# Kernel tuning notes

Hardware: AMD Instinct MI355X
Metric: run time of the kernel (lower is better)

The kernel has to match this reference:

```python
import jax, jax.numpy as jnp
import numpy as np

DIM = 1024
HEADS = 16
HEAD_DIM = DIM // HEADS
HIDDEN = 4 * DIM
EPS = 1e-6


def _layer_norm(x, scale, bias):
    mu = jnp.mean(x, axis=-1, keepdims=True)
    var = jnp.mean(jnp.square(x - mu), axis=-1, keepdims=True)
    return (x - mu) * jax.lax.rsqrt(var + EPS) * scale + bias


def setup_inputs() -> dict:
    key = jax.random.key(0)
    ks = jax.random.split(key, 8)
    s = 0.02
    return {
        "x": jax.random.normal(ks[0], (8, 1024, DIM), dtype=jnp.float32),
        "w_qkv": jax.random.normal(ks[1], (DIM, 3 * DIM), dtype=jnp.float32) * s,
        "b_qkv": jnp.zeros((3 * DIM,), jnp.float32),
        "w_proj": jax.random.normal(ks[2], (DIM, DIM), dtype=jnp.float32) * s,
        "b_proj": jnp.zeros((DIM,), jnp.float32),
        "ln1_scale": jnp.ones((DIM,), jnp.float32),
        "ln1_bias": jnp.zeros((DIM,), jnp.float32),
        "ln2_scale": jnp.ones((DIM,), jnp.float32),
        "ln2_bias": jnp.zeros((DIM,), jnp.float32),
        "w_fc1": jax.random.normal(ks[3], (DIM, HIDDEN), dtype=jnp.float32) * s,
        "b_fc1": jnp.zeros((HIDDEN,), jnp.float32),
        "w_fc2": jax.random.normal(ks[4], (HIDDEN, DIM), dtype=jnp.float32) * s,
        "b_fc2": jnp.zeros((DIM,), jnp.float32),
    }


def reference(x, w_qkv, b_qkv, w_proj, b_proj, ln1_scale, ln1_bias,
              ln2_scale, ln2_bias, w_fc1, b_fc1, w_fc2, b_fc2):
    B, N, C = x.shape
    scale = HEAD_DIM ** -0.5

    # --- attention branch ---
    h = _layer_norm(x, ln1_scale, ln1_bias)
    qkv = h @ w_qkv + b_qkv                          # [B,N,3C]
    qkv = qkv.reshape(B, N, 3, HEADS, HEAD_DIM)
    qkv = jnp.transpose(qkv, (2, 0, 3, 1, 4))        # [3,B,H,N,D]
    q, k, v = qkv[0], qkv[1], qkv[2]
    attn = jnp.einsum("bhnd,bhmd->bhnm", q, k) * scale
    attn = jax.nn.softmax(attn, axis=-1)
    o = jnp.einsum("bhnm,bhmd->bhnd", attn, v)       # [B,H,N,D]
    o = jnp.transpose(o, (0, 2, 1, 3)).reshape(B, N, C)
    x = x + (o @ w_proj + b_proj)

    # --- mlp branch ---
    h = _layer_norm(x, ln2_scale, ln2_bias)
    h = jax.nn.gelu(h @ w_fc1 + b_fc1)               # tanh approx, matches flax default
    x = x + (h @ w_fc2 + b_fc2)
    return x
```

## Files before the change

### kernel.cpp

```cpp
#include <hip/hip_runtime.h>

typedef __attribute__((ext_vector_type(8))) short short8;
typedef __attribute__((ext_vector_type(4))) float f32x4;
typedef unsigned short ushort;
typedef unsigned int uint;

#define DIM 1024
#define NSEQ 1024
#define BATCH 8
#define HEADS 16
#define HD 64
#define HIDDEN 4096
#define NROWS (BATCH * NSEQ)

__device__ inline ushort f2bf(float f) {
  uint u = __float_as_uint(f);
  u += 0x7fff + ((u >> 16) & 1);
  return (ushort)(u >> 16);
}

__device__ inline f32x4 zero4() {
  f32x4 z; z[0] = 0.f; z[1] = 0.f; z[2] = 0.f; z[3] = 0.f; return z;
}

__device__ inline float gelu_fast(float x) {
  float u2 = 1.5957691216057308f * (x + 0.044715f * x * x * x);
  float e = __builtin_amdgcn_exp2f(-1.4426950408889634f * u2);
  return x / (1.0f + e);
}

#define GLDS16(g, l)                                                  \
  __builtin_amdgcn_global_load_lds(                                   \
      (const __attribute__((address_space(1))) void*)(g),             \
      (__attribute__((address_space(3))) void*)(l), 16, 0, 0)

__global__ __launch_bounds__(256) void ln_kernel(
    const float* __restrict__ x, const float* __restrict__ sc,
    const float* __restrict__ bi, ushort* __restrict__ out) {
  int row = blockIdx.x;
  int t = threadIdx.x;
  const float4 v = reinterpret_cast<const float4*>(x + (size_t)row * DIM)[t];
  float s = v.x + v.y + v.z + v.w;
  float s2 = v.x * v.x + v.y * v.y + v.z * v.z + v.w * v.w;
#pragma unroll
  for (int off = 32; off >= 1; off >>= 1) {
    s += __shfl_xor(s, off);
    s2 += __shfl_xor(s2, off);
  }
  __shared__ float ps[4], ps2[4];
  int w = t >> 6;
  if ((t & 63) == 0) { ps[w] = s; ps2[w] = s2; }
  __syncthreads();
  s = ps[0] + ps[1] + ps[2] + ps[3];
  s2 = ps2[0] + ps2[1] + ps2[2] + ps2[3];
  float mu = s * (1.0f / DIM);
  float var = s2 * (1.0f / DIM) - mu * mu;
  float rstd = rsqrtf(var + 1e-6f);
  float4 scv = reinterpret_cast<const float4*>(sc)[t];
  float4 biv = reinterpret_cast<const float4*>(bi)[t];
  ushort4 o;
  o.x = f2bf((v.x - mu) * rstd * scv.x + biv.x);
  o.y = f2bf((v.y - mu) * rstd * scv.y + biv.y);
  o.z = f2bf((v.z - mu) * rstd * scv.z + biv.z);
  o.w = f2bf((v.w - mu) * rstd * scv.w + biv.w);
  reinterpret_cast<ushort4*>(out + (size_t)row * DIM)[t] = o;
}

__global__ __launch_bounds__(256) void wtrans_kernel(
    const float* __restrict__ w, ushort* __restrict__ wt, int K, int N) {
  __shared__ float tile[32][33];
  int n0 = blockIdx.x * 32, k0 = blockIdx.y * 32;
  int tx = threadIdx.x & 31, ty = threadIdx.x >> 5;
#pragma unroll
  for (int j = 0; j < 4; j++)
    tile[ty + 8 * j][tx] = w[(size_t)(k0 + ty + 8 * j) * N + n0 + tx];
  __syncthreads();
#pragma unroll
  for (int j = 0; j < 4; j++)
    wt[(size_t)(n0 + ty + 8 * j) * K + k0 + tx] = f2bf(tile[tx][ty + 8 * j]);
}

__global__ __launch_bounds__(256) void vtrans_kernel(
    const ushort* __restrict__ qkv, ushort* __restrict__ vT) {
  __shared__ ushort Ts[64 * 64];
  int bh = blockIdx.y;
  int b = bh >> 4, h = bh & 15;
  int n0 = blockIdx.x * 64;
  int t = threadIdx.x;
  const ushort* src = qkv + (size_t)b * NSEQ * 3072 + 2048 + h * 64;
#pragma unroll
  for (int i = 0; i < 2; i++) {
    int ci = i * 256 + t;
    int rr = ci >> 3, c = ci & 7;
    short8 v = *reinterpret_cast<const short8*>(src + (size_t)(n0 + rr) * 3072 + c * 8);
    *reinterpret_cast<short8*>(&Ts[rr * 64 + ((c ^ (rr >> 3)) & 7) * 8]) = v;
  }
  __syncthreads();
  ushort* dst = vT + (size_t)bh * 64 * NSEQ;
#pragma unroll
  for (int i = 0; i < 2; i++) {
    int ci = i * 256 + t;
    int dd = ci >> 3, c = ci & 7;
    short8 v;
#pragma unroll
    for (int j = 0; j < 8; j++) {
      int nn = c * 8 + j;
      v[j] = (short)Ts[nn * 64 + (((dd >> 3) ^ (nn >> 3)) & 7) * 8 + (dd & 7)];
    }
    *reinterpret_cast<short8*>(dst + (size_t)dd * NSEQ + n0 + c * 8) = v;
  }
}

template <int EPI>
__global__ __launch_bounds__(256, 3) void gemm128_kernel(
    const ushort* __restrict__ A, const ushort* __restrict__ Bt,
    const float* __restrict__ bias, const float* __restrict__ res,
    void* __restrict__ outp, int M, int N, int K) {
  constexpr int BM = 128, BN = 128, BK = 32;

  __shared__ ushort As[2][BM * BK];
  __shared__ ushort Bs[2][BN * BK];

  int t = threadIdx.x, lane = t & 63, w = t >> 6;
  int wr = w >> 1, wc = w & 1;
  int r = lane & 15, g = lane >> 4;

  int nwg = gridDim.x * gridDim.y;
  int flat = blockIdx.y * gridDim.x + blockIdx.x;
  int swzf = (flat & 7) * (nwg >> 3) + (flat >> 3);
  int bx = swzf % gridDim.x, by = swzf / gridDim.x;
  int m0 = by * BM, n0 = bx * BN;

  const ushort* Ab = A + (size_t)m0 * K;
  const ushort* Bb = Bt + (size_t)n0 * K;

  int srow = t >> 2;
  int sgc8 = (((t & 3) ^ (srow & 3) ^ ((srow >> 2) & 3)) & 3) * 8;
  int swb = (t >> 6) * 16 * BK;
  int sw = ((g ^ (r & 3) ^ ((r >> 2) & 3)) & 3) * 8;

  f32x4 acc[4][4];
#pragma unroll
  for (int mi = 0; mi < 4; mi++)
#pragma unroll
    for (int ni = 0; ni < 4; ni++) acc[mi][ni] = zero4();

  int nkt = K / BK;
#pragma unroll
  for (int p = 0; p < 2; p++) {
    GLDS16(Ab + (size_t)(p * 64 + srow) * K + sgc8, &As[0][(p * 64) * BK + swb]);
    GLDS16(Bb + (size_t)(p * 64 + srow) * K + sgc8, &Bs[0][(p * 64) * BK + swb]);
  }
  __syncthreads();

  int cur = 0;
  for (int kt = 0; kt < nkt; kt++) {
    if (kt + 1 < nkt) {
      int ko = (kt + 1) * BK;
#pragma unroll
      for (int p = 0; p < 2; p++) {
        GLDS16(Ab + (size_t)(p * 64 + srow) * K + ko + sgc8,
               &As[cur ^ 1][(p * 64) * BK + swb]);
        GLDS16(Bb + (size_t)(p * 64 + srow) * K + ko + sgc8,
               &Bs[cur ^ 1][(p * 64) * BK + swb]);
      }
    }
    short8 a[4], b[4];
#pragma unroll
    for (int mi = 0; mi < 4; mi++)
      a[mi] = *reinterpret_cast<const short8*>(
          &As[cur][(wr * 64 + mi * 16 + r) * BK + sw]);
#pragma unroll
    for (int ni = 0; ni < 4; ni++)
      b[ni] = *reinterpret_cast<const short8*>(
          &Bs[cur][(wc * 64 + ni * 16 + r) * BK + sw]);
#pragma unroll
    for (int mi = 0; mi < 4; mi++)
#pragma unroll
      for (int ni = 0; ni < 4; ni++)
        acc[mi][ni] = __builtin_amdgcn_mfma_f32_16x16x32_bf16(
            a[mi], b[ni], acc[mi][ni], 0, 0, 0);
    __syncthreads();
    cur ^= 1;
  }

  int rg = g * 4;
#pragma unroll
  for (int mi = 0; mi < 4; mi++) {
#pragma unroll
    for (int ni = 0; ni < 4; ni++) {
      int row = m0 + wr * 64 + mi * 16 + rg;
      int col = n0 + wc * 64 + ni * 16 + r;
      float bv = bias[col];
#pragma unroll
      for (int j = 0; j < 4; j++) {
        float v = acc[mi][ni][j] + bv;
        if (EPI == 1) v = gelu_fast(v);
        if (EPI == 2) {
          reinterpret_cast<float*>(outp)[(size_t)(row + j) * N + col] =
              v + res[(size_t)(row + j) * N + col];
        } else {
          reinterpret_cast<ushort*>(outp)[(size_t)(row + j) * N + col] = f2bf(v);
        }
      }
    }
  }
}

#define SM_SCALE_L2E 0.18033688f
#define SM_BIAS_L2E 11.54156036f
__global__ __launch_bounds__(256) void attn_kernel(
    const ushort* __restrict__ qkv, const ushort* __restrict__ vT,
    ushort* __restrict__ o) {
  __shared__ ushort Kt[64 * 72];
  __shared__ ushort Vt[64 * 72];
  __shared__ ushort Pl[4][16 * 72];
  int q0 = blockIdx.x * 64, h = blockIdx.y, b = blockIdx.z;
  int t = threadIdx.x, lane = t & 63, w = t >> 6;
  int r = lane & 15, g = lane >> 4;
  const ushort* base = qkv + (size_t)b * NSEQ * 3072 + h * 64;
  const ushort* vbase = vT + (size_t)(b * HEADS + h) * 64 * NSEQ;

  short8 qf[2];
  {
    const ushort* qrow = base + (size_t)(q0 + w * 16 + r) * 3072;
    qf[0] = *reinterpret_cast<const short8*>(qrow + g * 8);
    qf[1] = *reinterpret_cast<const short8*>(qrow + 32 + g * 8);
  }

  float l[4] = {0.f, 0.f, 0.f, 0.f};
  f32x4 oacc[4];
#pragma unroll
  for (int db = 0; db < 4; db++) oacc[db] = zero4();

  int srw = t >> 3, sc8 = (t & 7) * 8;
  for (int kt = 0; kt < NSEQ / 64; kt++) {
    int k0 = kt * 64;
    short8 kreg[2], vreg[2];
#pragma unroll
    for (int i = 0; i < 2; i++) {
      int rw = srw + i * 32;
      kreg[i] = *reinterpret_cast<const short8*>(base + 1024 + (size_t)(k0 + rw) * 3072 + sc8);
      vreg[i] = *reinterpret_cast<const short8*>(vbase + (size_t)rw * NSEQ + k0 + sc8);
    }
    __syncthreads();
#pragma unroll
    for (int i = 0; i < 2; i++) {
      int rw = srw + i * 32;
      *reinterpret_cast<short8*>(&Kt[rw * 72 + sc8]) = kreg[i];
      *reinterpret_cast<short8*>(&Vt[rw * 72 + sc8]) = vreg[i];
    }
    __syncthreads();

#pragma unroll
    for (int kb = 0; kb < 4; kb++) {
      short8 kf0 = *reinterpret_cast<const short8*>(&Kt[(kb * 16 + r) * 72 + g * 8]);
      short8 kf1 = *reinterpret_cast<const short8*>(&Kt[(kb * 16 + r) * 72 + 32 + g * 8]);
      f32x4 z = zero4();
      z = __builtin_amdgcn_mfma_f32_16x16x32_bf16(qf[0], kf0, z, 0, 0, 0);
      z = __builtin_amdgcn_mfma_f32_16x16x32_bf16(qf[1], kf1, z, 0, 0, 0);
#pragma unroll
      for (int j = 0; j < 4; j++) {
        float p = __builtin_amdgcn_exp2f(fmaf(z[j], SM_SCALE_L2E, -SM_BIAS_L2E));
        l[j] += p;
        Pl[w][(g * 4 + j) * 72 + kb * 16 + r] = (ushort)(__float_as_uint(p) >> 16);
      }
    }

#pragma unroll
    for (int ks = 0; ks < 2; ks++) {
      short8 pa = *reinterpret_cast<const short8*>(&Pl[w][r * 72 + ks * 32 + g * 8]);
#pragma unroll
      for (int db = 0; db < 4; db++) {
        short8 vb = *reinterpret_cast<const short8*>(&Vt[(db * 16 + r) * 72 + ks * 32 + g * 8]);
        oacc[db] = __builtin_amdgcn_mfma_f32_16x16x32_bf16(pa, vb, oacc[db], 0, 0, 0);
      }
    }
  }

#pragma unroll
  for (int j = 0; j < 4; j++) {
#pragma unroll
    for (int off = 8; off >= 1; off >>= 1) l[j] += __shfl_xor(l[j], off);
    l[j] = 1.0f / l[j];
  }

#pragma unroll
  for (int db = 0; db < 4; db++)
#pragma unroll
    for (int j = 0; j < 4; j++) {
      size_t row = (size_t)b * NSEQ + q0 + w * 16 + g * 4 + j;
      int col = h * 64 + db * 16 + r;
      o[row * DIM + col] = f2bf(oacc[db][j] * l[j]);
    }
}

extern "C" void kernel_launch(void* const* d_in, const int* in_sizes, int n_in,
                              void* d_out, int out_size, void* d_ws, size_t ws_size,
                              hipStream_t stream) {
  const float* x      = (const float*)d_in[0];
  const float* w_qkv  = (const float*)d_in[1];
  const float* b_qkv  = (const float*)d_in[2];
  const float* w_proj = (const float*)d_in[3];
  const float* b_proj = (const float*)d_in[4];
  const float* ln1s   = (const float*)d_in[5];
  const float* ln1b   = (const float*)d_in[6];
  const float* ln2s   = (const float*)d_in[7];
  const float* ln2b   = (const float*)d_in[8];
  const float* w_fc1  = (const float*)d_in[9];
  const float* b_fc1  = (const float*)d_in[10];
  const float* w_fc2  = (const float*)d_in[11];
  const float* b_fc2  = (const float*)d_in[12];
  float* out = (float*)d_out;

  char* ws = (char*)d_ws;
  ushort* wqkv_t  = (ushort*)(ws);
  ushort* wproj_t = (ushort*)(ws + 6291456);
  ushort* wfc1_t  = (ushort*)(ws + 8388608);
  ushort* wfc2_t  = (ushort*)(ws + 16777216);
  ushort* hbuf    = (ushort*)(ws + 25165824);
  float*  x1      = (float*)(ws + 41943040);
  ushort* vTb     = (ushort*)(ws + 41943040);
  ushort* qkv     = (ushort*)(ws + 75497472);
  ushort* obuf    = (ushort*)(ws + 125829120);
  ushort* fc1a    = qkv;

  wtrans_kernel<<<dim3(3072 / 32, 1024 / 32), 256, 0, stream>>>(w_qkv, wqkv_t, 1024, 3072);
  wtrans_kernel<<<dim3(1024 / 32, 1024 / 32), 256, 0, stream>>>(w_proj, wproj_t, 1024, 1024);
  wtrans_kernel<<<dim3(4096 / 32, 1024 / 32), 256, 0, stream>>>(w_fc1, wfc1_t, 1024, 4096);
  wtrans_kernel<<<dim3(1024 / 32, 4096 / 32), 256, 0, stream>>>(w_fc2, wfc2_t, 4096, 1024);

  ln_kernel<<<NROWS, 256, 0, stream>>>(x, ln1s, ln1b, hbuf);
  gemm128_kernel<0><<<dim3(3072 / 128, NROWS / 128), 256, 0, stream>>>(
      hbuf, wqkv_t, b_qkv, nullptr, qkv, NROWS, 3072, 1024);
  vtrans_kernel<<<dim3(NSEQ / 64, BATCH * HEADS), 256, 0, stream>>>(qkv, vTb);
  attn_kernel<<<dim3(NSEQ / 64, HEADS, BATCH), 256, 0, stream>>>(qkv, vTb, obuf);
  gemm128_kernel<2><<<dim3(1024 / 128, NROWS / 128), 256, 0, stream>>>(
      obuf, wproj_t, b_proj, x, x1, NROWS, 1024, 1024);

  ln_kernel<<<NROWS, 256, 0, stream>>>(x1, ln2s, ln2b, hbuf);
  gemm128_kernel<1><<<dim3(4096 / 128, NROWS / 128), 256, 0, stream>>>(
      hbuf, wfc1_t, b_fc1, nullptr, fc1a, NROWS, 4096, 1024);
  gemm128_kernel<2><<<dim3(1024 / 128, NROWS / 128), 256, 0, stream>>>(
      fc1a, wfc2_t, b_fc2, x1, out, NROWS, 1024, 4096);
}
```

Before: 414.4 us.

## Replace 128x128 GEMM with 256x256 8-wave ping-pong pipelined GEMM

Swaps the 128x128x32 double-buffered GEMM for a 256x256x64 tile kernel run by 512 threads. The K loop is split into four quadrant phases that interleave LDS fragment loads, async global-to-LDS staging up to two k-tiles ahead, and MFMA bursts raised with s_setprio, using explicit vmcnt waits and barriers. The aim is more data reuse per tile and hiding global latency behind MFMA work. In exchange it uses more registers and LDS (2 blocks/CU), and the small N=1024 GEMMs launch only 128 workgroups, which may underfill the GPU.

```diff
diff --git a/kernel.cpp b/kernel.cpp
--- a/kernel.cpp
+++ b/kernel.cpp
@@ -33,6 +33,13 @@
   __builtin_amdgcn_global_load_lds(                                   \
       (const __attribute__((address_space(1))) void*)(g),             \
       (__attribute__((address_space(3))) void*)(l), 16, 0, 0)
+
+#define WAITVM(n) asm volatile("s_waitcnt vmcnt(" #n ")" ::: "memory")
+#define SBAR() asm volatile("s_barrier" ::: "memory")
+#define LGKM0() do {                                            \
+    asm volatile("s_waitcnt lgkmcnt(0)" ::: "memory");          \
+    __builtin_amdgcn_sched_barrier(0);                          \
+  } while (0)
 
 __global__ __launch_bounds__(256) void ln_kernel(
     const float* __restrict__ x, const float* __restrict__ sc,
@@ -112,17 +119,16 @@
 }
 
 template <int EPI>
-__global__ __launch_bounds__(256, 3) void gemm128_kernel(
+__global__ __launch_bounds__(512, 2) void gemm256p_kernel(
     const ushort* __restrict__ A, const ushort* __restrict__ Bt,
     const float* __restrict__ bias, const float* __restrict__ res,
     void* __restrict__ outp, int M, int N, int K) {
-  constexpr int BM = 128, BN = 128, BK = 32;
-
-  __shared__ ushort As[2][BM * BK];
-  __shared__ ushort Bs[2][BN * BK];
+  constexpr int BM = 256, BN = 256, BK = 64;
+  __shared__ ushort As[2][2][128 * 64];
+  __shared__ ushort Bs[2][2][128 * 64];
 
   int t = threadIdx.x, lane = t & 63, w = t >> 6;
-  int wr = w >> 1, wc = w & 1;
+  int wr = w >> 2, wc = w & 3;
   int r = lane & 15, g = lane >> 4;
 
   int nwg = gridDim.x * gridDim.y;
@@ -134,62 +140,142 @@
   const ushort* Ab = A + (size_t)m0 * K;
   const ushort* Bb = Bt + (size_t)n0 * K;
 
-  int srow = t >> 2;
-  int sgc8 = (((t & 3) ^ (srow & 3) ^ ((srow >> 2) & 3)) & 3) * 8;
-  int swb = (t >> 6) * 16 * BK;
-  int sw = ((g ^ (r & 3) ^ ((r >> 2) & 3)) & 3) * 8;
-
-  f32x4 acc[4][4];
-#pragma unroll
-  for (int mi = 0; mi < 4; mi++)
+  int srow = t >> 3;
+  int scg8 = ((t & 7) ^ ((t >> 5) & 3)) * 8;
+  int sdst = w * 512;
+  int rchunk8 = (g ^ ((r >> 2) & 3)) * 8;
+
+  auto stageA = [&](int kt2, int h) {
+    const ushort* src = Ab + (size_t)(h * 128 + srow) * K + kt2 * 64 + scg8;
+    ushort* dst = &As[kt2 & 1][h][sdst];
+    GLDS16(src, dst);
+    GLDS16(src + (size_t)64 * K, dst + 4096);
+  };
+  auto stageB = [&](int kt2, int h) {
+    const ushort* src = Bb + (size_t)(h * 128 + srow) * K + kt2 * 64 + scg8;
+    ushort* dst = &Bs[kt2 & 1][h][sdst];
+    GLDS16(src, dst);
+    GLDS16(src + (size_t)64 * K, dst + 4096);
+  };
+
+  f32x4 acc[8][4];
+#pragma unroll
+  for (int mi = 0; mi < 8; mi++)
 #pragma unroll
     for (int ni = 0; ni < 4; ni++) acc[mi][ni] = zero4();
 
-  int nkt = K / BK;
-#pragma unroll
-  for (int p = 0; p < 2; p++) {
-    GLDS16(Ab + (size_t)(p * 64 + srow) * K + sgc8, &As[0][(p * 64) * BK + swb]);
-    GLDS16(Bb + (size_t)(p * 64 + srow) * K + sgc8, &Bs[0][(p * 64) * BK + swb]);
-  }
-  __syncthreads();
-
-  int cur = 0;
+  const int nkt = K / BK;
+  const int hb = wc >> 1;
+  const int rowB0 = (wc & 1) * 64;
+
+  stageA(0, 0); stageA(0, 1); stageB(0, 0); stageB(0, 1);
+  stageB(1, 0); stageA(1, 0);
+  WAITVM(4);
+  SBAR();
+
+  short8 aQ[4][2], bQ0[2][2], bQ1[2][2];
+
+#pragma unroll 1
   for (int kt = 0; kt < nkt; kt++) {
-    if (kt + 1 < nkt) {
-      int ko = (kt + 1) * BK;
-#pragma unroll
-      for (int p = 0; p < 2; p++) {
-        GLDS16(Ab + (size_t)(p * 64 + srow) * K + ko + sgc8,
-               &As[cur ^ 1][(p * 64) * BK + swb]);
-        GLDS16(Bb + (size_t)(p * 64 + srow) * K + ko + sgc8,
-               &Bs[cur ^ 1][(p * 64) * BK + swb]);
-      }
-    }
-    short8 a[4], b[4];
-#pragma unroll
-    for (int mi = 0; mi < 4; mi++)
-      a[mi] = *reinterpret_cast<const short8*>(
-          &As[cur][(wr * 64 + mi * 16 + r) * BK + sw]);
-#pragma unroll
-    for (int ni = 0; ni < 4; ni++)
-      b[ni] = *reinterpret_cast<const short8*>(
-          &Bs[cur][(wc * 64 + ni * 16 + r) * BK + sw]);
-#pragma unroll
-    for (int mi = 0; mi < 4; mi++)
-#pragma unroll
-      for (int ni = 0; ni < 4; ni++)
-        acc[mi][ni] = __builtin_amdgcn_mfma_f32_16x16x32_bf16(
-            a[mi], b[ni], acc[mi][ni], 0, 0, 0);
-    __syncthreads();
-    cur ^= 1;
+    const ushort* as = &As[kt & 1][wr][0];
+    const ushort* bs = &Bs[kt & 1][hb][0];
+
+#pragma unroll
+    for (int i = 0; i < 4; i++)
+#pragma unroll
+      for (int ks = 0; ks < 2; ks++)
+        aQ[i][ks] = *reinterpret_cast<const short8*>(
+            &as[(i * 16 + r) * 64 + ks * 32 + rchunk8]);
+#pragma unroll
+    for (int n2 = 0; n2 < 2; n2++)
+#pragma unroll
+      for (int ks = 0; ks < 2; ks++)
+        bQ0[n2][ks] = *reinterpret_cast<const short8*>(
+            &bs[(rowB0 + n2 * 16 + r) * 64 + ks * 32 + rchunk8]);
+    if (kt + 1 < nkt) stageA(kt + 1, 1);
+    SBAR();
+    LGKM0();
+    __builtin_amdgcn_s_setprio(1);
+#pragma unroll
+    for (int i = 0; i < 4; i++)
+#pragma unroll
+      for (int n2 = 0; n2 < 2; n2++)
+#pragma unroll
+        for (int ks = 0; ks < 2; ks++)
+          acc[i][n2] = __builtin_amdgcn_mfma_f32_16x16x32_bf16(
+              aQ[i][ks], bQ0[n2][ks], acc[i][n2], 0, 0, 0);
+    __builtin_amdgcn_s_setprio(0);
+    SBAR();
+
+#pragma unroll
+    for (int n2 = 0; n2 < 2; n2++)
+#pragma unroll
+      for (int ks = 0; ks < 2; ks++)
+        bQ1[n2][ks] = *reinterpret_cast<const short8*>(
+            &bs[(rowB0 + 32 + n2 * 16 + r) * 64 + ks * 32 + rchunk8]);
+    if (kt + 1 < nkt) stageB(kt + 1, 1);
+    SBAR();
+    LGKM0();
+    __builtin_amdgcn_s_setprio(1);
+#pragma unroll
+    for (int i = 0; i < 4; i++)
+#pragma unroll
+      for (int n2 = 0; n2 < 2; n2++)
+#pragma unroll
+        for (int ks = 0; ks < 2; ks++)
+          acc[i][2 + n2] = __builtin_amdgcn_mfma_f32_16x16x32_bf16(
+              aQ[i][ks], bQ1[n2][ks], acc[i][2 + n2], 0, 0, 0);
+    __builtin_amdgcn_s_setprio(0);
+    SBAR();
+
+#pragma unroll
+    for (int i = 0; i < 4; i++)
+#pragma unroll
+      for (int ks = 0; ks < 2; ks++)
+        aQ[i][ks] = *reinterpret_cast<const short8*>(
+            &as[(64 + i * 16 + r) * 64 + ks * 32 + rchunk8]);
+    if (kt + 2 < nkt) stageB(kt + 2, 0);
+    SBAR();
+    LGKM0();
+    __builtin_amdgcn_s_setprio(1);
+#pragma unroll
+    for (int i = 0; i < 4; i++)
+#pragma unroll
+      for (int n2 = 0; n2 < 2; n2++)
+#pragma unroll
+        for (int ks = 0; ks < 2; ks++)
+          acc[4 + i][2 + n2] = __builtin_amdgcn_mfma_f32_16x16x32_bf16(
+              aQ[i][ks], bQ1[n2][ks], acc[4 + i][2 + n2], 0, 0, 0);
+    __builtin_amdgcn_s_setprio(0);
+    SBAR();
+
+    if (kt + 2 < nkt) stageA(kt + 2, 0);
+    SBAR();
+    __builtin_amdgcn_s_setprio(1);
+#pragma unroll
+    for (int i = 0; i < 4; i++)
+#pragma unroll
+      for (int n2 = 0; n2 < 2; n2++)
+#pragma unroll
+        for (int ks = 0; ks < 2; ks++)
+          acc[4 + i][n2] = __builtin_amdgcn_mfma_f32_16x16x32_bf16(
+              aQ[i][ks], bQ0[n2][ks], acc[4 + i][n2], 0, 0, 0);
+    __builtin_amdgcn_s_setprio(0);
+    if (kt + 2 < nkt) {
+      WAITVM(4);
+      SBAR();
+    } else if (kt + 1 < nkt) {
+      WAITVM(0);
+      SBAR();
+    }
   }
 
   int rg = g * 4;
 #pragma unroll
-  for (int mi = 0; mi < 4; mi++) {
+  for (int mi = 0; mi < 8; mi++) {
 #pragma unroll
     for (int ni = 0; ni < 4; ni++) {
-      int row = m0 + wr * 64 + mi * 16 + rg;
+      int row = m0 + wr * 128 + mi * 16 + rg;
       int col = n0 + wc * 64 + ni * 16 + r;
       float bv = bias[col];
 #pragma unroll
@@ -331,16 +417,16 @@
   wtrans_kernel<<<dim3(1024 / 32, 4096 / 32), 256, 0, stream>>>(w_fc2, wfc2_t, 4096, 1024);
 
   ln_kernel<<<NROWS, 256, 0, stream>>>(x, ln1s, ln1b, hbuf);
-  gemm128_kernel<0><<<dim3(3072 / 128, NROWS / 128), 256, 0, stream>>>(
+  gemm256p_kernel<0><<<dim3(3072 / 256, NROWS / 256), 512, 0, stream>>>(
       hbuf, wqkv_t, b_qkv, nullptr, qkv, NROWS, 3072, 1024);
   vtrans_kernel<<<dim3(NSEQ / 64, BATCH * HEADS), 256, 0, stream>>>(qkv, vTb);
   attn_kernel<<<dim3(NSEQ / 64, HEADS, BATCH), 256, 0, stream>>>(qkv, vTb, obuf);
-  gemm128_kernel<2><<<dim3(1024 / 128, NROWS / 128), 256, 0, stream>>>(
+  gemm256p_kernel<2><<<dim3(1024 / 256, NROWS / 256), 512, 0, stream>>>(
       obuf, wproj_t, b_proj, x, x1, NROWS, 1024, 1024);
 
   ln_kernel<<<NROWS, 256, 0, stream>>>(x1, ln2s, ln2b, hbuf);
-  gemm128_kernel<1><<<dim3(4096 / 128, NROWS / 128), 256, 0, stream>>>(
+  gemm256p_kernel<1><<<dim3(4096 / 256, NROWS / 256), 512, 0, stream>>>(
       hbuf, wfc1_t, b_fc1, nullptr, fc1a, NROWS, 4096, 1024);
-  gemm128_kernel<2><<<dim3(1024 / 128, NROWS / 128), 256, 0, stream>>>(
+  gemm256p_kernel<2><<<dim3(1024 / 256, NROWS / 256), 512, 0, stream>>>(
       fc1a, wfc2_t, b_fc2, x1, out, NROWS, 1024, 4096);
 }
```

After: 503.2 us. 21.4% more time.
